# Performance work log

Hardware: AMD Instinct MI355X
Metric: run time of the kernel (lower is better)

Reference implementation:

```python
import jax, jax.numpy as jnp
import numpy as np

B, C, H, W = 32, 384, 28, 28
E, HID, K = 4, 384, 2  # HID = hidden_features(1536) // num_experts(4)


def setup_inputs() -> dict:
    key = jax.random.key(0)
    ks = jax.random.split(key, 5)
    x = jax.random.normal(ks[0], (B, C, H, W), jnp.float32)
    gate_w = jax.random.normal(ks[1], (C, E), jnp.float32) * 0.02
    gate_b = jnp.zeros((E,), jnp.float32)
    w1 = jax.random.normal(ks[2], (E, HID, C), jnp.float32) * 0.02
    b1 = jnp.zeros((E, HID), jnp.float32)
    w2 = jax.random.normal(ks[3], (E, C, HID), jnp.float32) * 0.02
    b2 = jnp.zeros((E, C), jnp.float32)
    return {"x": x, "gate_w": gate_w, "gate_b": gate_b,
            "w1": w1, "b1": b1, "w2": w2, "b2": b2}


def reference(x, gate_w, gate_b, w1, b1, w2, b2):
    b, c, h, w = x.shape
    e = gate_b.shape[0]
    # per-token gating: tokens are spatial positions in NHWC order
    x_flat = x.transpose(0, 2, 3, 1).reshape(-1, c)          # [N, C], N = B*H*W
    scores = jax.nn.softmax(x_flat @ gate_w + gate_b, -1)    # [N, E]
    top_v, top_i = jax.lax.top_k(scores, K)                  # [N, K]
    top_w = jax.nn.softmax(top_v, -1)                        # [N, K] renormalized
    # weight map per top-k slot: [K, B, H, W]
    wmap = top_w.T.reshape(K, b, h, w)
    # faithful to torch loop: expert i contributes at slot k iff ANY token routed
    # to it at slot k; the weight applied is the UNMASKED slot-k weight map.
    present = (top_i[:, :, None] == jnp.arange(e)[None, None, :]).any(0)  # [K, E]
    coef = jnp.einsum('ke,kbhw->ebhw', present.astype(x.dtype), wmap)     # [E, B, H, W]
    # dense per-expert 1x1-conv MLP over the FULL tensor (as in the source)
    hdn = jax.nn.relu(jnp.einsum('bchw,edc->ebdhw', x, w1)
                      + b1[:, None, :, None, None])          # [E, B, HID, H, W]
    y = jnp.einsum('ebdhw,eod->ebohw', hdn, w2) + b2[:, None, :, None, None]
    out = jnp.einsum('ebohw,ebhw->bohw', y, coef)            # [B, C, H, W]
    return out
```

## Files before the change

kernel.cpp:

```cpp
#include <hip/hip_runtime.h>
#include <hip/hip_bf16.h>
#include <stdint.h>

#define B_DIM 32
#define C_DIM 384
#define HW_DIM 784
#define E_DIM 4
#define HID_DIM 384
#define NTOK (B_DIM * HW_DIM)
#define NH (E_DIM * HID_DIM)
#define WSZ 589824

using short8 = __attribute__((ext_vector_type(8))) short;
using f32x4  = __attribute__((ext_vector_type(4))) float;
typedef unsigned short ushort_t;

__device__ __forceinline__ ushort_t f2bf(float f) {
  __hip_bfloat16 h = __float2bfloat16(f);
  return __builtin_bit_cast(ushort_t, h);
}

__device__ __forceinline__ void gload_lds16(const void* g, void* l) {
  __builtin_amdgcn_global_load_lds(
      (const __attribute__((address_space(1))) unsigned int*)g,
      (__attribute__((address_space(3))) unsigned int*)l, 16, 0, 0);
}

__global__ __launch_bounds__(256) void prep_kernel(
    const float* __restrict__ w1, const float* __restrict__ w2,
    ushort_t* __restrict__ W1f, ushort_t* __restrict__ W2f,
    unsigned int* __restrict__ present) {
  int i = blockIdx.x * 256 + threadIdx.x;
  if (i == 0) *present = 0u;
  if (i >= WSZ) return;
  {
    int r = i;
    const int nt = r / 49152; r -= nt * 49152;
    const int ks = r / 4096;  r -= ks * 4096;
    const int wn = r >> 11;
    const int ni = (r >> 9) & 3;
    const int ln = (r >> 3) & 63;
    const int tt = r & 7;
    const int row = nt * 128 + wn * 64 + ni * 16 + (ln & 15);
    const int c = ks * 32 + (ln >> 4) * 8 + tt;
    W1f[i] = f2bf(w1[(size_t)row * C_DIM + c]);
  }
  {
    int r = i;
    const int nt = r / 196608; r -= nt * 196608;
    const int ks = r / 4096;   r -= ks * 4096;
    const int wn = r >> 11;
    const int ni = (r >> 9) & 3;
    const int ln = (r >> 3) & 63;
    const int tt = r & 7;
    const int o = nt * 128 + wn * 64 + ni * 16 + (ln & 15);
    const int kg = ks * 32 + (ln >> 4) * 8 + tt;
    const int e = kg / HID_DIM, d = kg - e * HID_DIM;
    W2f[i] = f2bf(w2[((size_t)e * C_DIM + o) * HID_DIM + d]);
  }
}

__global__ __launch_bounds__(512) void gate_kernel(
    const float* __restrict__ x, const float* __restrict__ gw,
    const float* __restrict__ gb, ushort_t* __restrict__ xb,
    float* __restrict__ topw, unsigned int* __restrict__ present) {
  __shared__ __align__(16) ushort_t lxs[64][392];
  __shared__ float pscore[8][64][4];
  __shared__ unsigned int pmask;
  const int b = blockIdx.x;
  const int p0 = blockIdx.y * 64;
  const int cnt = min(64, HW_DIM - p0);
  const int tid = threadIdx.x;
  const int cg = tid >> 6, tl = tid & 63;
  if (tid == 0) pmask = 0u;
  float a0 = 0.f, a1 = 0.f, a2 = 0.f, a3 = 0.f;
  const bool valid = tl < cnt;
  if (valid) {
    const float* xp = x + (size_t)b * C_DIM * HW_DIM + p0 + tl;
    for (int c = cg; c < C_DIM; c += 8) {
      const float v = xp[(size_t)c * HW_DIM];
      lxs[tl][c] = f2bf(v);
      const float4 g = *(const float4*)&gw[c * 4];
      a0 += v * g.x; a1 += v * g.y; a2 += v * g.z; a3 += v * g.w;
    }
  }
  pscore[cg][tl][0] = a0; pscore[cg][tl][1] = a1;
  pscore[cg][tl][2] = a2; pscore[cg][tl][3] = a3;
  __syncthreads();
  if (cg == 0 && valid) {
    float z[4];
#pragma unroll
    for (int e = 0; e < 4; e++) {
      float s = gb[e];
#pragma unroll
      for (int g8 = 0; g8 < 8; g8++) s += pscore[g8][tl][e];
      z[e] = s;
    }
    const float mx = fmaxf(fmaxf(z[0], z[1]), fmaxf(z[2], z[3]));
    float s[4]; float sum = 0.f;
#pragma unroll
    for (int e = 0; e < 4; e++) { s[e] = __expf(z[e] - mx); sum += s[e]; }
    const float inv = 1.f / sum;
#pragma unroll
    for (int e = 0; e < 4; e++) s[e] *= inv;
    int e0 = 0; float v0 = s[0];
#pragma unroll
    for (int e = 1; e < 4; e++) if (s[e] > v0) { v0 = s[e]; e0 = e; }
    int e1 = -1; float v1 = -1.f;
#pragma unroll
    for (int e = 0; e < 4; e++) if (e != e0 && s[e] > v1) { v1 = s[e]; e1 = e; }
    const float r = __expf(v1 - v0);
    const float w0 = 1.f / (1.f + r);
    const int m = b * HW_DIM + p0 + tl;
    topw[m * 2] = w0;
    topw[m * 2 + 1] = 1.f - w0;
    atomicOr(&pmask, (1u << e0) | (1u << (4 + e1)));
  }
  __syncthreads();
  if (tid == 0) atomicOr(present, pmask);
  const int nchunk = cnt * 48;
  for (int ci = tid; ci < nchunk; ci += 512) {
    const int row = ci / 48, c8 = ci - row * 48;
    short8 v = *(const short8*)&lxs[row][c8 * 8];
    *(short8*)&xb[(size_t)(b * HW_DIM + p0 + row) * C_DIM + c8 * 8] = v;
  }
}

template <int KDIM, int EPI>
__global__ __launch_bounds__(256, 3) void gemm_bg(
    const ushort_t* __restrict__ A, const ushort_t* __restrict__ Wf,
    const float* __restrict__ bias, const float* __restrict__ topw,
    const unsigned int* __restrict__ presentp,
    ushort_t* __restrict__ hOut, float* __restrict__ outp) {
  constexpr int BM = 128, BN = 128, BK = 32;
  constexpr int KT = KDIM / BK;
  constexpr int NTN = (EPI == 0 ? NH / BN : C_DIM / BN);
  constexpr int ASZ = BM * BK;
  __shared__ ushort_t smem[3 * ASZ];

  const int nwg = NTN * (NTOK / BM);
  const int orig = blockIdx.x;
  const int xcd = orig & 7;
  const int qq = nwg >> 3, rr = nwg & 7;
  const int wg = (xcd < rr ? xcd * (qq + 1) : rr * (qq + 1) + (xcd - rr) * qq)
               + (orig >> 3);
  const int mt = wg / NTN, nt = wg % NTN;
  const int m0 = mt * BM, n0 = nt * BN;

  const int tid = threadIdx.x;
  const int lane = tid & 63;
  const int wid = tid >> 6;
  const int wm = wid >> 1, wn = wid & 1;
  const int lanel = lane & 15, laneq = lane >> 4;

  const ushort_t* wbase = Wf + (size_t)nt * KT * 4096 + wn * 2048 + lane * 8;

  auto stage = [&](int t) {
    ushort_t* dstA = smem + (t % 3) * ASZ;
    const int kb = t * BK;
#pragma unroll
    for (int li = 0; li < 2; ++li) {
      const int P = (li * 256 + tid) * 16;
      const int row = P >> 6;
      const int cb = (P & 63) ^ (((row >> 1) & 3) << 4);
      gload_lds16(&A[(size_t)(m0 + row) * KDIM + kb + (cb >> 1)],
                  (char*)dstA + P);
    }
  };

  auto loadB = [&](int t, short8* bv) {
    const ushort_t* p = wbase + (size_t)t * 4096;
    asm volatile(
        "global_load_dwordx4 %0, %4, off\n\t"
        "global_load_dwordx4 %1, %4, off offset:1024\n\t"
        "global_load_dwordx4 %2, %4, off offset:2048\n\t"
        "global_load_dwordx4 %3, %4, off offset:3072"
        : "=&v"(bv[0]), "=&v"(bv[1]), "=&v"(bv[2]), "=&v"(bv[3])
        : "v"(p)
        : "memory");
  };

  f32x4 acc[4][4] = {};
  const int cbr = (laneq * 16) ^ (((lanel >> 1) & 3) << 4);

  short8 bvA[4], bvB[4];

  auto step = [&](int t, short8* cur, short8* nxt) {
    if (t + 1 < KT)
      asm volatile("s_waitcnt vmcnt(2)" ::: "memory");
    else
      asm volatile("s_waitcnt vmcnt(0)" ::: "memory");
    __builtin_amdgcn_sched_barrier(0);
    __builtin_amdgcn_s_barrier();
    __builtin_amdgcn_sched_barrier(0);
    if (t + 1 < KT) loadB(t + 1, nxt);
    __builtin_amdgcn_sched_barrier(0);
    if (t + 2 < KT) stage(t + 2);
    const char* Ab =
        (const char*)(smem + (t % 3) * ASZ) + (wm * 64 + lanel) * 64;
    short8 av[4];
#pragma unroll
    for (int i = 0; i < 4; ++i) av[i] = *(const short8*)(Ab + i * 1024 + cbr);
    __builtin_amdgcn_s_setprio(1);
#pragma unroll
    for (int i = 0; i < 4; ++i)
#pragma unroll
      for (int j = 0; j < 4; ++j)
        acc[i][j] = __builtin_amdgcn_mfma_f32_16x16x32_bf16(
            av[i], cur[j], acc[i][j], 0, 0, 0);
    __builtin_amdgcn_s_setprio(0);
  };

  stage(0);
  loadB(0, bvA);
  stage(1);
  for (int t = 0; t < KT; t += 2) {
    step(t, bvA, bvB);
    step(t + 1, bvB, bvA);
  }

  const unsigned int pm = *presentp;
  if constexpr (EPI == 0) {
    __syncthreads();
    ushort_t* tr = smem;
    const int e = n0 / HID_DIM;
    const float P0 = (float)((pm >> e) & 1u);
    const float P1 = (float)((pm >> (4 + e)) & 1u);
#pragma unroll
    for (int s = 0; s < 2; ++s) {
      if (wm == s) {
#pragma unroll
        for (int mi = 0; mi < 4; ++mi) {
          const int r0 = mi * 16 + laneq * 4;
          const int mg = m0 + s * 64 + r0;
          const float4 t0 = *(const float4*)&topw[mg * 2];
          const float4 t1 = *(const float4*)&topw[mg * 2 + 4];
          const float cj[4] = {P0 * t0.x + P1 * t0.y, P0 * t0.z + P1 * t0.w,
                               P0 * t1.x + P1 * t1.y, P0 * t1.z + P1 * t1.w};
#pragma unroll
          for (int ni = 0; ni < 4; ++ni) {
            const int cl = wn * 64 + ni * 16 + lanel;
            const float bvv = bias[n0 + cl];
#pragma unroll
            for (int j = 0; j < 4; ++j) {
              float v = fmaxf(acc[mi][ni][j] + bvv, 0.f);
              tr[(r0 + j) * 128 + cl] = f2bf(cj[j] * v);
            }
          }
        }
      }
      __syncthreads();
#pragma unroll
      for (int it = 0; it < 4; ++it) {
        const int c = it * 256 + tid;
        const int row = c >> 4, cr = c & 15;
        *(short8*)&hOut[(size_t)(m0 + s * 64 + row) * NH + n0 + cr * 8] =
            *(const short8*)&tr[row * 128 + cr * 8];
      }
      __syncthreads();
    }
  } else {
    float B0[4], B1[4];
#pragma unroll
    for (int ni = 0; ni < 4; ++ni) {
      const int o = n0 + wn * 64 + ni * 16 + lanel;
      float s0 = 0.f, s1 = 0.f;
#pragma unroll
      for (int e2 = 0; e2 < 4; ++e2) {
        const float bb = bias[e2 * C_DIM + o];
        s0 += (float)((pm >> e2) & 1u) * bb;
        s1 += (float)((pm >> (4 + e2)) & 1u) * bb;
      }
      B0[ni] = s0; B1[ni] = s1;
    }
#pragma unroll
    for (int mi = 0; mi < 4; ++mi) {
      const int mg = m0 + wm * 64 + mi * 16 + laneq * 4;
      const float4 t0 = *(const float4*)&topw[mg * 2];
      const float4 t1 = *(const float4*)&topw[mg * 2 + 4];
      const int bb2 = mg / HW_DIM;
      const int p = mg - bb2 * HW_DIM;
#pragma unroll
      for (int ni = 0; ni < 4; ++ni) {
        const int o = n0 + wn * 64 + ni * 16 + lanel;
        float4 v;
        v.x = acc[mi][ni][0] + t0.x * B0[ni] + t0.y * B1[ni];
        v.y = acc[mi][ni][1] + t0.z * B0[ni] + t0.w * B1[ni];
        v.z = acc[mi][ni][2] + t1.x * B0[ni] + t1.y * B1[ni];
        v.w = acc[mi][ni][3] + t1.z * B0[ni] + t1.w * B1[ni];
        *(float4*)&outp[((size_t)bb2 * C_DIM + o) * HW_DIM + p] = v;
      }
    }
  }
}

extern "C" void kernel_launch(void* const* d_in, const int* in_sizes, int n_in,
                              void* d_out, int out_size, void* d_ws, size_t ws_size,
                              hipStream_t stream) {
  const float* x  = (const float*)d_in[0];
  const float* gw = (const float*)d_in[1];
  const float* gb = (const float*)d_in[2];
  const float* w1 = (const float*)d_in[3];
  const float* b1 = (const float*)d_in[4];
  const float* w2 = (const float*)d_in[5];
  const float* b2 = (const float*)d_in[6];
  float* out = (float*)d_out;

  char* ws = (char*)d_ws;
  ushort_t* xb = (ushort_t*)ws;   ws += (size_t)NTOK * C_DIM * 2;
  ushort_t* hdnS = (ushort_t*)ws; ws += (size_t)NTOK * NH * 2;
  ushort_t* W1f = (ushort_t*)ws;  ws += (size_t)WSZ * 2;
  ushort_t* W2f = (ushort_t*)ws;  ws += (size_t)WSZ * 2;
  float* topw = (float*)ws;       ws += (size_t)NTOK * 2 * 4;
  unsigned int* present = (unsigned int*)ws;

  prep_kernel<<<dim3(WSZ / 256), dim3(256), 0, stream>>>(
      w1, w2, W1f, W2f, present);
  gate_kernel<<<dim3(B_DIM, 13), dim3(512), 0, stream>>>(
      x, gw, gb, xb, topw, present);
  gemm_bg<C_DIM, 0>
      <<<dim3((NTOK / 128) * (NH / 128)), dim3(256), 0, stream>>>(
          xb, W1f, b1, topw, present, hdnS, nullptr);
  gemm_bg<NH, 1>
      <<<dim3((NTOK / 128) * (C_DIM / 128)), dim3(256), 0, stream>>>(
          hdnS, W2f, b2, topw, present, nullptr, out);
}
```

Measured before the change: 120.1 us.

## Replace LDS-staged 128x128 GEMM with single-wave 64x64 register-direct GEMM

Both GEMMs now use one 64-thread wave per 64x64 output tile. A and B fragments are loaded straight from global memory into registers with double buffering, so the LDS staging and the per-step workgroup barriers are gone. The epilogue uses a smaller swizzled LDS tile for the transposed bf16 store. The trade-off is 4x more workgroups and half the reuse of each loaded A/B element, which raises global and L2 traffic and loses the async LDS prefetch pipeline.

After: 182.3 us. 1.52x slower.

```diff
diff --git a/kernel.cpp b/kernel.cpp
--- a/kernel.cpp
+++ b/kernel.cpp
@@ -18,12 +18,6 @@
 __device__ __forceinline__ ushort_t f2bf(float f) {
   __hip_bfloat16 h = __float2bfloat16(f);
   return __builtin_bit_cast(ushort_t, h);
-}
-
-__device__ __forceinline__ void gload_lds16(const void* g, void* l) {
-  __builtin_amdgcn_global_load_lds(
-      (const __attribute__((address_space(1))) unsigned int*)g,
-      (__attribute__((address_space(3))) unsigned int*)l, 16, 0, 0);
 }
 
 __global__ __launch_bounds__(256) void prep_kernel(
@@ -127,143 +121,105 @@
 }
 
 template <int KDIM, int EPI>
-__global__ __launch_bounds__(256, 3) void gemm_bg(
+__global__ __launch_bounds__(64, 3) void gemm_nl(
     const ushort_t* __restrict__ A, const ushort_t* __restrict__ Wf,
     const float* __restrict__ bias, const float* __restrict__ topw,
     const unsigned int* __restrict__ presentp,
     ushort_t* __restrict__ hOut, float* __restrict__ outp) {
-  constexpr int BM = 128, BN = 128, BK = 32;
-  constexpr int KT = KDIM / BK;
-  constexpr int NTN = (EPI == 0 ? NH / BN : C_DIM / BN);
-  constexpr int ASZ = BM * BK;
-  __shared__ ushort_t smem[3 * ASZ];
-
-  const int nwg = NTN * (NTOK / BM);
+  constexpr int KT = KDIM / 32;
+  constexpr int NTN = (EPI == 0 ? NH / 64 : C_DIM / 64);
+  __shared__ __align__(16) ushort_t tr[64 * 64];
+
+  const int nwg = NTN * (NTOK / 64);
   const int orig = blockIdx.x;
   const int xcd = orig & 7;
   const int qq = nwg >> 3, rr = nwg & 7;
   const int wg = (xcd < rr ? xcd * (qq + 1) : rr * (qq + 1) + (xcd - rr) * qq)
                + (orig >> 3);
   const int mt = wg / NTN, nt = wg % NTN;
-  const int m0 = mt * BM, n0 = nt * BN;
-
-  const int tid = threadIdx.x;
-  const int lane = tid & 63;
-  const int wid = tid >> 6;
-  const int wm = wid >> 1, wn = wid & 1;
+  const int m0 = mt * 64, n0 = nt * 64;
+
+  const int lane = threadIdx.x;
   const int lanel = lane & 15, laneq = lane >> 4;
 
-  const ushort_t* wbase = Wf + (size_t)nt * KT * 4096 + wn * 2048 + lane * 8;
-
-  auto stage = [&](int t) {
-    ushort_t* dstA = smem + (t % 3) * ASZ;
-    const int kb = t * BK;
-#pragma unroll
-    for (int li = 0; li < 2; ++li) {
-      const int P = (li * 256 + tid) * 16;
-      const int row = P >> 6;
-      const int cb = (P & 63) ^ (((row >> 1) & 3) << 4);
-      gload_lds16(&A[(size_t)(m0 + row) * KDIM + kb + (cb >> 1)],
-                  (char*)dstA + P);
-    }
+  const ushort_t* Abase = A + (size_t)(m0 + lanel) * KDIM + laneq * 8;
+  const ushort_t* Bbase =
+      Wf + (size_t)(nt >> 1) * KT * 4096 + (nt & 1) * 2048 + lane * 8;
+
+  f32x4 acc[4][4] = {};
+  short8 avA[4], bvA[4], avB[4], bvB[4];
+
+  auto ldA = [&](int t, short8* av) {
+    const ushort_t* p = Abase + t * 32;
+#pragma unroll
+    for (int i = 0; i < 4; ++i)
+      av[i] = *(const short8*)(p + (size_t)i * 16 * KDIM);
   };
-
-  auto loadB = [&](int t, short8* bv) {
-    const ushort_t* p = wbase + (size_t)t * 4096;
-    asm volatile(
-        "global_load_dwordx4 %0, %4, off\n\t"
-        "global_load_dwordx4 %1, %4, off offset:1024\n\t"
-        "global_load_dwordx4 %2, %4, off offset:2048\n\t"
-        "global_load_dwordx4 %3, %4, off offset:3072"
-        : "=&v"(bv[0]), "=&v"(bv[1]), "=&v"(bv[2]), "=&v"(bv[3])
-        : "v"(p)
-        : "memory");
+  auto ldB = [&](int t, short8* bv) {
+    const ushort_t* p = Bbase + (size_t)t * 4096;
+#pragma unroll
+    for (int j = 0; j < 4; ++j) bv[j] = *(const short8*)(p + j * 512);
   };
-
-  f32x4 acc[4][4] = {};
-  const int cbr = (laneq * 16) ^ (((lanel >> 1) & 3) << 4);
-
-  short8 bvA[4], bvB[4];
-
-  auto step = [&](int t, short8* cur, short8* nxt) {
-    if (t + 1 < KT)
-      asm volatile("s_waitcnt vmcnt(2)" ::: "memory");
-    else
-      asm volatile("s_waitcnt vmcnt(0)" ::: "memory");
-    __builtin_amdgcn_sched_barrier(0);
-    __builtin_amdgcn_s_barrier();
-    __builtin_amdgcn_sched_barrier(0);
-    if (t + 1 < KT) loadB(t + 1, nxt);
-    __builtin_amdgcn_sched_barrier(0);
-    if (t + 2 < KT) stage(t + 2);
-    const char* Ab =
-        (const char*)(smem + (t % 3) * ASZ) + (wm * 64 + lanel) * 64;
-    short8 av[4];
-#pragma unroll
-    for (int i = 0; i < 4; ++i) av[i] = *(const short8*)(Ab + i * 1024 + cbr);
+  auto mfma16 = [&](short8* av, short8* bv) {
     __builtin_amdgcn_s_setprio(1);
 #pragma unroll
     for (int i = 0; i < 4; ++i)
 #pragma unroll
       for (int j = 0; j < 4; ++j)
         acc[i][j] = __builtin_amdgcn_mfma_f32_16x16x32_bf16(
-            av[i], cur[j], acc[i][j], 0, 0, 0);
+            av[i], bv[j], acc[i][j], 0, 0, 0);
     __builtin_amdgcn_s_setprio(0);
   };
 
-  stage(0);
-  loadB(0, bvA);
-  stage(1);
+  ldA(0, avA); ldB(0, bvA);
+  ldA(1, avB); ldB(1, bvB);
   for (int t = 0; t < KT; t += 2) {
-    step(t, bvA, bvB);
-    step(t + 1, bvB, bvA);
+    mfma16(avA, bvA);
+    if (t + 2 < KT) { ldA(t + 2, avA); ldB(t + 2, bvA); }
+    mfma16(avB, bvB);
+    if (t + 3 < KT) { ldA(t + 3, avB); ldB(t + 3, bvB); }
   }
 
   const unsigned int pm = *presentp;
   if constexpr (EPI == 0) {
-    __syncthreads();
-    ushort_t* tr = smem;
     const int e = n0 / HID_DIM;
     const float P0 = (float)((pm >> e) & 1u);
     const float P1 = (float)((pm >> (4 + e)) & 1u);
 #pragma unroll
-    for (int s = 0; s < 2; ++s) {
-      if (wm == s) {
-#pragma unroll
-        for (int mi = 0; mi < 4; ++mi) {
-          const int r0 = mi * 16 + laneq * 4;
-          const int mg = m0 + s * 64 + r0;
-          const float4 t0 = *(const float4*)&topw[mg * 2];
-          const float4 t1 = *(const float4*)&topw[mg * 2 + 4];
-          const float cj[4] = {P0 * t0.x + P1 * t0.y, P0 * t0.z + P1 * t0.w,
-                               P0 * t1.x + P1 * t1.y, P0 * t1.z + P1 * t1.w};
-#pragma unroll
-          for (int ni = 0; ni < 4; ++ni) {
-            const int cl = wn * 64 + ni * 16 + lanel;
-            const float bvv = bias[n0 + cl];
-#pragma unroll
-            for (int j = 0; j < 4; ++j) {
-              float v = fmaxf(acc[mi][ni][j] + bvv, 0.f);
-              tr[(r0 + j) * 128 + cl] = f2bf(cj[j] * v);
-            }
-          }
+    for (int mi = 0; mi < 4; ++mi) {
+      const int r0 = mi * 16 + laneq * 4;
+      const int mg = m0 + r0;
+      const float4 t0 = *(const float4*)&topw[mg * 2];
+      const float4 t1 = *(const float4*)&topw[mg * 2 + 4];
+      const float cj[4] = {P0 * t0.x + P1 * t0.y, P0 * t0.z + P1 * t0.w,
+                           P0 * t1.x + P1 * t1.y, P0 * t1.z + P1 * t1.w};
+#pragma unroll
+      for (int ni = 0; ni < 4; ++ni) {
+        const int cl = ni * 16 + lanel;
+        const float bvv = bias[n0 + cl];
+#pragma unroll
+        for (int j = 0; j < 4; ++j) {
+          const int row = r0 + j;
+          float v = fmaxf(acc[mi][ni][j] + bvv, 0.f);
+          *(ushort_t*)((char*)tr + row * 128 + ((cl * 2) ^ ((row & 7) << 4))) =
+              f2bf(cj[j] * v);
         }
       }
-      __syncthreads();
-#pragma unroll
-      for (int it = 0; it < 4; ++it) {
-        const int c = it * 256 + tid;
-        const int row = c >> 4, cr = c & 15;
-        *(short8*)&hOut[(size_t)(m0 + s * 64 + row) * NH + n0 + cr * 8] =
-            *(const short8*)&tr[row * 128 + cr * 8];
-      }
-      __syncthreads();
+    }
+    __syncthreads();
+#pragma unroll
+    for (int it = 0; it < 8; ++it) {
+      const int c = it * 64 + lane;
+      const int row = c >> 3, cc = c & 7;
+      short8 v = *(const short8*)((char*)tr + row * 128 +
+                                  ((cc * 16) ^ ((row & 7) << 4)));
+      *(short8*)&hOut[(size_t)(m0 + row) * NH + n0 + cc * 8] = v;
     }
   } else {
     float B0[4], B1[4];
 #pragma unroll
     for (int ni = 0; ni < 4; ++ni) {
-      const int o = n0 + wn * 64 + ni * 16 + lanel;
+      const int o = n0 + ni * 16 + lanel;
       float s0 = 0.f, s1 = 0.f;
 #pragma unroll
       for (int e2 = 0; e2 < 4; ++e2) {
@@ -275,14 +231,14 @@
     }
 #pragma unroll
     for (int mi = 0; mi < 4; ++mi) {
-      const int mg = m0 + wm * 64 + mi * 16 + laneq * 4;
+      const int mg = m0 + mi * 16 + laneq * 4;
       const float4 t0 = *(const float4*)&topw[mg * 2];
       const float4 t1 = *(const float4*)&topw[mg * 2 + 4];
       const int bb2 = mg / HW_DIM;
       const int p = mg - bb2 * HW_DIM;
 #pragma unroll
       for (int ni = 0; ni < 4; ++ni) {
-        const int o = n0 + wn * 64 + ni * 16 + lanel;
+        const int o = n0 + ni * 16 + lanel;
         float4 v;
         v.x = acc[mi][ni][0] + t0.x * B0[ni] + t0.y * B1[ni];
         v.y = acc[mi][ni][1] + t0.z * B0[ni] + t0.w * B1[ni];
@@ -318,10 +274,10 @@
       w1, w2, W1f, W2f, present);
   gate_kernel<<<dim3(B_DIM, 13), dim3(512), 0, stream>>>(
       x, gw, gb, xb, topw, present);
-  gemm_bg<C_DIM, 0>
-      <<<dim3((NTOK / 128) * (NH / 128)), dim3(256), 0, stream>>>(
+  gemm_nl<C_DIM, 0>
+      <<<dim3((NTOK / 64) * (NH / 64)), dim3(64), 0, stream>>>(
           xb, W1f, b1, topw, present, hdnS, nullptr);
-  gemm_bg<NH, 1>
-      <<<dim3((NTOK / 128) * (C_DIM / 128)), dim3(256), 0, stream>>>(
+  gemm_nl<NH, 1>
+      <<<dim3((NTOK / 64) * (C_DIM / 64)), dim3(64), 0, stream>>>(
           hdnS, W2f, b2, topw, present, nullptr, out);
 }
```

## Use two-wave 128-thread GEMM blocks with 128x64 warp tiles and deeper B prefetch

Applied to the files above, without the earlier changes.

The GEMM block shrinks from 4 waves to 2. Each wave now covers all 128 rows and 64 columns, giving 8x4 accumulator tiles per wave, which doubles register reuse of the B fragments and halves redundant B global loads per tile. B loads move from inline asm to plain loads with a two-step-ahead prefetch, and the vmcnt waits are adjusted to match. The cost is many more accumulator VGPRs, which may limit occupancy to 2 blocks. Fewer waves per CU are left to hide LDS and global latency.

After: 118.6 us. No clear change (-1.3%).

```diff
diff --git a/kernel.cpp b/kernel.cpp
--- a/kernel.cpp
+++ b/kernel.cpp
@@ -127,7 +127,7 @@
 }
 
 template <int KDIM, int EPI>
-__global__ __launch_bounds__(256, 3) void gemm_bg(
+__global__ __launch_bounds__(128, 2) void gemm_bd(
     const ushort_t* __restrict__ A, const ushort_t* __restrict__ Wf,
     const float* __restrict__ bias, const float* __restrict__ topw,
     const unsigned int* __restrict__ presentp,
@@ -149,74 +149,65 @@
 
   const int tid = threadIdx.x;
   const int lane = tid & 63;
-  const int wid = tid >> 6;
-  const int wm = wid >> 1, wn = wid & 1;
+  const int wn = tid >> 6;
   const int lanel = lane & 15, laneq = lane >> 4;
 
   const ushort_t* wbase = Wf + (size_t)nt * KT * 4096 + wn * 2048 + lane * 8;
 
   auto stage = [&](int t) {
-    ushort_t* dstA = smem + (t % 3) * ASZ;
+    ushort_t* dst = smem + (t % 3) * ASZ;
     const int kb = t * BK;
 #pragma unroll
-    for (int li = 0; li < 2; ++li) {
-      const int P = (li * 256 + tid) * 16;
+    for (int li = 0; li < 4; ++li) {
+      const int P = (li * 128 + tid) * 16;
       const int row = P >> 6;
       const int cb = (P & 63) ^ (((row >> 1) & 3) << 4);
       gload_lds16(&A[(size_t)(m0 + row) * KDIM + kb + (cb >> 1)],
-                  (char*)dstA + P);
+                  (char*)dst + P);
     }
   };
-
-  auto loadB = [&](int t, short8* bv) {
+  auto ldB = [&](int t, short8* bv) {
     const ushort_t* p = wbase + (size_t)t * 4096;
-    asm volatile(
-        "global_load_dwordx4 %0, %4, off\n\t"
-        "global_load_dwordx4 %1, %4, off offset:1024\n\t"
-        "global_load_dwordx4 %2, %4, off offset:2048\n\t"
-        "global_load_dwordx4 %3, %4, off offset:3072"
-        : "=&v"(bv[0]), "=&v"(bv[1]), "=&v"(bv[2]), "=&v"(bv[3])
-        : "v"(p)
-        : "memory");
+#pragma unroll
+    for (int j = 0; j < 4; ++j) bv[j] = *(const short8*)(p + j * 512);
   };
 
-  f32x4 acc[4][4] = {};
+  f32x4 acc[8][4] = {};
   const int cbr = (laneq * 16) ^ (((lanel >> 1) & 3) << 4);
 
   short8 bvA[4], bvB[4];
 
-  auto step = [&](int t, short8* cur, short8* nxt) {
+  auto step = [&](int t, short8* cur) {
     if (t + 1 < KT)
-      asm volatile("s_waitcnt vmcnt(2)" ::: "memory");
+      asm volatile("s_waitcnt vmcnt(10)" ::: "memory");
     else
-      asm volatile("s_waitcnt vmcnt(0)" ::: "memory");
+      asm volatile("s_waitcnt vmcnt(4)" ::: "memory");
     __builtin_amdgcn_sched_barrier(0);
     __builtin_amdgcn_s_barrier();
     __builtin_amdgcn_sched_barrier(0);
-    if (t + 1 < KT) loadB(t + 1, nxt);
-    __builtin_amdgcn_sched_barrier(0);
     if (t + 2 < KT) stage(t + 2);
-    const char* Ab =
-        (const char*)(smem + (t % 3) * ASZ) + (wm * 64 + lanel) * 64;
-    short8 av[4];
-#pragma unroll
-    for (int i = 0; i < 4; ++i) av[i] = *(const short8*)(Ab + i * 1024 + cbr);
+    const char* Ab = (const char*)(smem + (t % 3) * ASZ) + lanel * 64;
+    short8 av[8];
+#pragma unroll
+    for (int i = 0; i < 8; ++i) av[i] = *(const short8*)(Ab + i * 1024 + cbr);
     __builtin_amdgcn_s_setprio(1);
 #pragma unroll
-    for (int i = 0; i < 4; ++i)
+    for (int i = 0; i < 8; ++i)
 #pragma unroll
       for (int j = 0; j < 4; ++j)
         acc[i][j] = __builtin_amdgcn_mfma_f32_16x16x32_bf16(
             av[i], cur[j], acc[i][j], 0, 0, 0);
     __builtin_amdgcn_s_setprio(0);
+    if (t + 2 < KT) ldB(t + 2, cur);
   };
 
   stage(0);
-  loadB(0, bvA);
+  ldB(0, bvA);
   stage(1);
+  ldB(1, bvB);
   for (int t = 0; t < KT; t += 2) {
-    step(t, bvA, bvB);
-    step(t + 1, bvB, bvA);
+    step(t, bvA);
+    step(t + 1, bvB);
   }
 
   const unsigned int pm = *presentp;
@@ -228,31 +219,30 @@
     const float P1 = (float)((pm >> (4 + e)) & 1u);
 #pragma unroll
     for (int s = 0; s < 2; ++s) {
-      if (wm == s) {
-#pragma unroll
-        for (int mi = 0; mi < 4; ++mi) {
-          const int r0 = mi * 16 + laneq * 4;
-          const int mg = m0 + s * 64 + r0;
-          const float4 t0 = *(const float4*)&topw[mg * 2];
-          const float4 t1 = *(const float4*)&topw[mg * 2 + 4];
-          const float cj[4] = {P0 * t0.x + P1 * t0.y, P0 * t0.z + P1 * t0.w,
-                               P0 * t1.x + P1 * t1.y, P0 * t1.z + P1 * t1.w};
-#pragma unroll
-          for (int ni = 0; ni < 4; ++ni) {
-            const int cl = wn * 64 + ni * 16 + lanel;
-            const float bvv = bias[n0 + cl];
-#pragma unroll
-            for (int j = 0; j < 4; ++j) {
-              float v = fmaxf(acc[mi][ni][j] + bvv, 0.f);
-              tr[(r0 + j) * 128 + cl] = f2bf(cj[j] * v);
-            }
+#pragma unroll
+      for (int mi2 = 0; mi2 < 4; ++mi2) {
+        const int mi = s * 4 + mi2;
+        const int r0 = mi2 * 16 + laneq * 4;
+        const int mg = m0 + s * 64 + r0;
+        const float4 t0 = *(const float4*)&topw[mg * 2];
+        const float4 t1 = *(const float4*)&topw[mg * 2 + 4];
+        const float cj[4] = {P0 * t0.x + P1 * t0.y, P0 * t0.z + P1 * t0.w,
+                             P0 * t1.x + P1 * t1.y, P0 * t1.z + P1 * t1.w};
+#pragma unroll
+        for (int ni = 0; ni < 4; ++ni) {
+          const int cl = wn * 64 + ni * 16 + lanel;
+          const float bvv = bias[n0 + cl];
+#pragma unroll
+          for (int j = 0; j < 4; ++j) {
+            float v = fmaxf(acc[mi][ni][j] + bvv, 0.f);
+            tr[(r0 + j) * 128 + cl] = f2bf(cj[j] * v);
           }
         }
       }
       __syncthreads();
 #pragma unroll
-      for (int it = 0; it < 4; ++it) {
-        const int c = it * 256 + tid;
+      for (int it = 0; it < 8; ++it) {
+        const int c = it * 128 + tid;
         const int row = c >> 4, cr = c & 15;
         *(short8*)&hOut[(size_t)(m0 + s * 64 + row) * NH + n0 + cr * 8] =
             *(const short8*)&tr[row * 128 + cr * 8];
@@ -274,8 +264,8 @@
       B0[ni] = s0; B1[ni] = s1;
     }
 #pragma unroll
-    for (int mi = 0; mi < 4; ++mi) {
-      const int mg = m0 + wm * 64 + mi * 16 + laneq * 4;
+    for (int mi = 0; mi < 8; ++mi) {
+      const int mg = m0 + mi * 16 + laneq * 4;
       const float4 t0 = *(const float4*)&topw[mg * 2];
       const float4 t1 = *(const float4*)&topw[mg * 2 + 4];
       const int bb2 = mg / HW_DIM;
@@ -318,10 +308,10 @@
       w1, w2, W1f, W2f, present);
   gate_kernel<<<dim3(B_DIM, 13), dim3(512), 0, stream>>>(
       x, gw, gb, xb, topw, present);
-  gemm_bg<C_DIM, 0>
-      <<<dim3((NTOK / 128) * (NH / 128)), dim3(256), 0, stream>>>(
+  gemm_bd<C_DIM, 0>
+      <<<dim3((NTOK / 128) * (NH / 128)), dim3(128), 0, stream>>>(
           xb, W1f, b1, topw, present, hdnS, nullptr);
-  gemm_bg<NH, 1>
-      <<<dim3((NTOK / 128) * (C_DIM / 128)), dim3(256), 0, stream>>>(
+  gemm_bd<NH, 1>
+      <<<dim3((NTOK / 128) * (C_DIM / 128)), dim3(128), 0, stream>>>(
           hdnS, W2f, b2, topw, present, nullptr, out);
 }
```
